# Optimization experiments

Hardware: AMD Instinct MI355X
Metric: run time of the kernel (lower is better)

The kernel has to match this reference:

```python
import jax, jax.numpy as jnp
import numpy as np

IN_F, OUT_F = 768, 2304
E, R = 8, 16            # num adapters, lora rank
ALPHA = 32
SCALING = ALPHA / R
GATE_DIM = 64


def setup_inputs() -> dict:
    key = jax.random.key(0)
    ks = jax.random.split(key, 8)
    B, S = 8, 2048
    x = jax.random.normal(ks[0], (B, S, IN_F), dtype=jnp.float32)
    z = jax.random.normal(ks[1], (B, GATE_DIM), dtype=jnp.float32)
    # frozen linear (nn.Linear weight layout [out, in])
    W = jax.random.normal(ks[2], (OUT_F, IN_F), dtype=jnp.float32) * 0.02
    b = jax.random.normal(ks[3], (OUT_F,), dtype=jnp.float32) * 0.02
    # stacked LoRA adapters: A [E, r, in], B [E, out, r]
    A = jax.random.normal(ks[4], (E, R, IN_F), dtype=jnp.float32) * (1.0 / np.sqrt(IN_F))
    Bm = jax.random.normal(ks[5], (E, OUT_F, R), dtype=jnp.float32) * 0.02
    # spectral gate: linear + softmax over experts
    Wg = jax.random.normal(ks[6], (E, GATE_DIM), dtype=jnp.float32) * 0.1
    bg = jax.random.normal(ks[7], (E,), dtype=jnp.float32) * 0.1
    return {"x": x, "z": z, "W": W, "b": b, "A": A, "Bm": Bm, "Wg": Wg, "bg": bg}


def reference(x, z, W, b, A, Bm, Wg, bg):
    # frozen linear: [B,S,out]
    frozen_out = jnp.einsum('bsi,oi->bso', x, W) + b
    # gate weights over adapters: [B,E]
    gate_w = jax.nn.softmax(jnp.einsum('bg,eg->be', z, Wg) + bg, axis=-1)
    # fused adapters: down-proj to rank r per expert (dropout p=0 -> identity)
    h = jnp.einsum('bsi,eri->bser', x, A)               # [B,S,E,r] small (r=16)
    # up-proj + gate-weighted sum over experts, fused into one contraction
    adapt = jnp.einsum('bser,eor,be->bso', h, Bm, gate_w) * SCALING
    return frozen_out + adapt
```

## Files before the change

### kernel.cpp

```cpp
#include <hip/hip_runtime.h>
#include <hip/hip_bf16.h>
#include <stdint.h>

typedef unsigned short u16;
typedef __attribute__((ext_vector_type(8))) short short8;
typedef __attribute__((ext_vector_type(4))) float floatx4;
typedef unsigned int __attribute__((ext_vector_type(2))) uint2v;

#define M_TOT 16384
#define N_OUT 2304
#define KX    768
#define KL    128
#define SCALING 2.0f

#define WBLKS   864
#define ABLKS   48
#define BMRBLKS 144
#define PREP_BLOCKS (WBLKS + ABLKS + BMRBLKS + 1)

__device__ __forceinline__ u16 f2b(float f) {
  union { __hip_bfloat16 h; u16 u; } c; c.h = __float2bfloat16(f); return c.u;
}
__device__ __forceinline__ float ldf(const void* p, long i, bool f32) {
  if (f32) return ((const float*)p)[i];
  union { u16 u; __hip_bfloat16 h; } c; c.u = ((const u16*)p)[i];
  return __bfloat162float(c.h);
}

__device__ __forceinline__ void gload_lds16(const void* g, void* l) {
  __builtin_amdgcn_global_load_lds(
      (const __attribute__((address_space(1))) void*)g,
      (__attribute__((address_space(3))) void*)l, 16, 0, 0);
}

__device__ __forceinline__ void cvt8(const void* src, u16* dst, long i, bool f32) {
  u16 v[8];
  if (f32) {
    const float4* s = (const float4*)src;
    float4 a = s[i * 2], b = s[i * 2 + 1];
    v[0] = f2b(a.x); v[1] = f2b(a.y); v[2] = f2b(a.z); v[3] = f2b(a.w);
    v[4] = f2b(b.x); v[5] = f2b(b.y); v[6] = f2b(b.z); v[7] = f2b(b.w);
  } else {
    *(uint4*)v = ((const uint4*)src)[i];
  }
  ((uint4*)dst)[i] = *(uint4*)v;
}

__global__ __launch_bounds__(256) void prep_kernel(
    const void* __restrict__ x,  const void* __restrict__ W,
    const void* __restrict__ A,  const void* __restrict__ Bm,
    const void* __restrict__ z,  const void* __restrict__ Wg,
    const void* __restrict__ bg,
    u16* __restrict__ Wbf, u16* __restrict__ Abf,
    u16* __restrict__ bmr, float* __restrict__ gsc, int* __restrict__ flagp) {
  __shared__ int s_flag;
  const int tid = threadIdx.x;
  if (tid < 64) {
    u16 v = ((const u16*)x)[tid * 2];
    int e = (v >> 7) & 0xFF;
    int huge = (e >= 160) ? 1 : 0;
    for (int off = 1; off < 64; off <<= 1) huge += __shfl_xor(huge, off, 64);
    if (tid == 0) s_flag = (huge >= 4) ? 1 : 0;
  }
  __syncthreads();
  const bool f32 = (s_flag != 0);

  int b = blockIdx.x;
  if (b < WBLKS) {
    cvt8(W, Wbf, (long)b * 256 + tid, f32);
  } else if (b < WBLKS + ABLKS) {
    cvt8(A, Abf, (long)(b - WBLKS) * 256 + tid, f32);
  } else if (b < WBLKS + ABLKS + BMRBLKS) {
    long i0 = ((long)(b - WBLKS - ABLKS) * 256 + tid) * 8;
    u16 v[8];
#pragma unroll
    for (int j = 0; j < 8; ++j) {
      long idx = i0 + j;
      long o = idx >> 7, er = idx & 127;
      long e = er >> 4, r = er & 15;
      v[j] = f2b(ldf(Bm, (e * 2304 + o) * 16 + r, f32));
    }
    *(uint4*)&bmr[i0] = *(uint4*)v;
  } else {
    if (tid == 0) *flagp = s_flag;
    if (tid < 64) {
      const int bb = tid >> 3, e = tid & 7;
      float acc = ldf(bg, e, f32);
      for (int i = 0; i < 64; ++i)
        acc += ldf(z, bb * 64 + i, f32) * ldf(Wg, e * 64 + i, f32);
      float mx = acc;
      for (int off = 1; off < 8; off <<= 1) mx = fmaxf(mx, __shfl_xor(mx, off, 64));
      float ex = __expf(acc - mx);
      float sm = ex;
      for (int off = 1; off < 8; off <<= 1) sm += __shfl_xor(sm, off, 64);
      gsc[tid] = (ex / sm) * SCALING;
    }
  }
}

__global__ __launch_bounds__(256) void gemm_h(
    const void* __restrict__ x, const u16* __restrict__ Abf,
    const float* __restrict__ gsc, u16* __restrict__ xbf,
    u16* __restrict__ hg, const int* __restrict__ flagp) {
  __shared__ __align__(128) u16 As[64][64];
  __shared__ __align__(128) u16 Bs[128][64];
  const int tid = threadIdx.x, wave = tid >> 6, lane = tid & 63;
  const int wm = wave >> 1, wn = wave & 1;
  const int quad = lane >> 4, l16 = lane & 15;
  const int srow = lane >> 3, scol = (lane & 7) * 8;
  const int m0 = blockIdx.x * 64;
  const bool f32 = (*flagp != 0);

  const int xr = tid >> 2, cg16 = (tid & 3) * 16;
  char* Asb = (char*)&As[0][0];

  floatx4 acc[2][4];
#pragma unroll
  for (int i = 0; i < 2; ++i)
#pragma unroll
    for (int j = 0; j < 4; ++j) acc[i][j] = floatx4{0.f, 0.f, 0.f, 0.f};

  for (int kb = 0; kb < 12; ++kb) {
    const int kc = kb * 64;
    {
      const long off = (long)(m0 + xr) * KX + kc + cg16;
      uint4 lo, hi;
      if (f32) {
        const float4* xs = (const float4*)((const float*)x + off);
        float4 f0 = xs[0], f1 = xs[1], f2c = xs[2], f3 = xs[3];
        u16 v[16];
        v[0] = f2b(f0.x); v[1] = f2b(f0.y); v[2]  = f2b(f0.z); v[3]  = f2b(f0.w);
        v[4] = f2b(f1.x); v[5] = f2b(f1.y); v[6]  = f2b(f1.z); v[7]  = f2b(f1.w);
        v[8] = f2b(f2c.x); v[9] = f2b(f2c.y); v[10] = f2b(f2c.z); v[11] = f2b(f2c.w);
        v[12] = f2b(f3.x); v[13] = f2b(f3.y); v[14] = f2b(f3.z); v[15] = f2b(f3.w);
        lo = *(uint4*)&v[0]; hi = *(uint4*)&v[8];
      } else {
        lo = *(const uint4*)&((const u16*)x)[off];
        hi = *(const uint4*)&((const u16*)x)[off + 8];
      }
      *(uint4*)&xbf[off] = lo;
      *(uint4*)&xbf[off + 8] = hi;
      const int cb = cg16 * 2, sw = (xr & 7) << 4;
      *(uint4*)(Asb + xr * 128 + ((cb +  0) ^ sw)) = lo;
      *(uint4*)(Asb + xr * 128 + ((cb + 16) ^ sw)) = hi;
    }
#pragma unroll
    for (int j = 0; j < 4; ++j) {
      int r = wave * 32 + j * 8 + srow;
      gload_lds16(Abf + (size_t)r * KX + kc + scol,
                  (char*)(&Bs[0][0]) + (wave * 32 + j * 8) * 128);
    }
    __syncthreads();
#pragma unroll
    for (int ks = 0; ks < 2; ++ks) {
      short8 af[2], bf[4];
#pragma unroll
      for (int mi = 0; mi < 2; ++mi) {
        int ar = wm * 32 + mi * 16 + l16;
        af[mi] = *(const short8*)(Asb + ar * 128 + ((ks * 64 + quad * 16) ^ ((ar & 7) << 4)));
      }
#pragma unroll
      for (int ni = 0; ni < 4; ++ni)
        bf[ni] = *(const short8*)&Bs[wn * 64 + ni * 16 + l16][ks * 32 + quad * 8];
#pragma unroll
      for (int mi = 0; mi < 2; ++mi)
#pragma unroll
        for (int ni = 0; ni < 4; ++ni)
          acc[mi][ni] = __builtin_amdgcn_mfma_f32_16x16x32_bf16(af[mi], bf[ni], acc[mi][ni], 0, 0, 0);
    }
    __syncthreads();
  }
  const int bb = m0 >> 11;
  float gv[4];
#pragma unroll
  for (int ni = 0; ni < 4; ++ni) gv[ni] = gsc[bb * 8 + wn * 4 + ni];
#pragma unroll
  for (int mi = 0; mi < 2; ++mi) {
    int rbase = m0 + wm * 32 + mi * 16 + quad * 4;
#pragma unroll
    for (int ni = 0; ni < 4; ++ni) {
      int c = wn * 64 + ni * 16 + l16;
#pragma unroll
      for (int t = 0; t < 4; ++t)
        hg[(size_t)(rbase + t) * KL + c] = f2b(acc[mi][ni][t] * gv[ni]);
    }
  }
}

__global__ __launch_bounds__(256) void gemm_main(
    const u16* __restrict__ xbf, const u16* __restrict__ hg,
    const u16* __restrict__ Wbf, const u16* __restrict__ bmr,
    const void* __restrict__ bias, void* __restrict__ outv,
    const int* __restrict__ flagp) {
  __shared__ __align__(128) u16 As[128][64];
  __shared__ __align__(128) u16 Bs[128][64];
  __shared__ u16 occ_pad[4096];
  const int tid = threadIdx.x, wave = tid >> 6, lane = tid & 63;
  const int wm = wave >> 1, wn = wave & 1;
  const int quad = lane >> 4, l16 = lane & 15;
  const int srow = lane >> 3, scol = (lane & 7) * 8;

  const int linear = blockIdx.x;
  const int xcd = linear & 7;
  const int g = linear >> 3;
  const int st = g / 24;
  const int w  = g % 24;
  const int m_idx = xcd * 16 + (st / 6) * 8 + (w & 7);
  const int n_idx = (st % 6) * 3 + (w >> 3);
  const int m0 = m_idx * 128;
  const int n0 = n_idx * 128;
  if (tid == 0) ((volatile u16*)occ_pad)[0] = (u16)linear;

  floatx4 acc[4][4];
#pragma unroll
  for (int i = 0; i < 4; ++i)
#pragma unroll
    for (int j = 0; j < 4; ++j) acc[i][j] = floatx4{0.f, 0.f, 0.f, 0.f};

  for (int kb = 0; kb < 14; ++kb) {
    const u16* ap; const u16* bp; int lda, ldb, kc;
    if (kb < 12) { ap = xbf; lda = KX; bp = Wbf; ldb = KX; kc = kb * 64; }
    else         { ap = hg;  lda = KL; bp = bmr; ldb = KL; kc = (kb - 12) * 64; }
#pragma unroll
    for (int j = 0; j < 4; ++j) {
      int r = wave * 32 + j * 8 + srow;
      gload_lds16(ap + (size_t)(m0 + r) * lda + kc + scol,
                  (char*)(&As[0][0]) + (wave * 32 + j * 8) * 128);
      gload_lds16(bp + (size_t)(n0 + r) * ldb + kc + scol,
                  (char*)(&Bs[0][0]) + (wave * 32 + j * 8) * 128);
    }
    __syncthreads();
#pragma unroll
    for (int ks = 0; ks < 2; ++ks) {
      short8 af[4], bf[4];
#pragma unroll
      for (int mi = 0; mi < 4; ++mi)
        af[mi] = *(const short8*)&As[wm * 64 + mi * 16 + l16][ks * 32 + quad * 8];
#pragma unroll
      for (int ni = 0; ni < 4; ++ni)
        bf[ni] = *(const short8*)&Bs[wn * 64 + ni * 16 + l16][ks * 32 + quad * 8];
#pragma unroll
      for (int mi = 0; mi < 4; ++mi)
#pragma unroll
        for (int ni = 0; ni < 4; ++ni)
          acc[mi][ni] = __builtin_amdgcn_mfma_f32_16x16x32_bf16(bf[ni], af[mi], acc[mi][ni], 0, 0, 0);
    }
    __syncthreads();
  }

  const bool f32 = (*flagp != 0);
#pragma unroll
  for (int mi = 0; mi < 4; ++mi) {
    const size_t row = (size_t)(m0 + wm * 64 + mi * 16 + l16);
#pragma unroll
    for (int ni = 0; ni < 4; ++ni) {
      const int c0 = n0 + wn * 64 + ni * 16 + quad * 4;
      float b0, b1, b2, b3;
      if (f32) {
        const float4 bv = *(const float4*)((const float*)bias + c0);
        b0 = bv.x; b1 = bv.y; b2 = bv.z; b3 = bv.w;
      } else {
        b0 = ldf(bias, c0, false);     b1 = ldf(bias, c0 + 1, false);
        b2 = ldf(bias, c0 + 2, false); b3 = ldf(bias, c0 + 3, false);
      }
      const float v0 = acc[mi][ni][0] + b0, v1 = acc[mi][ni][1] + b1;
      const float v2 = acc[mi][ni][2] + b2, v3 = acc[mi][ni][3] + b3;
      if (f32) {
        floatx4 v = {v0, v1, v2, v3};
        __builtin_nontemporal_store(
            v, (floatx4*)((float*)outv + row * N_OUT + c0));
      } else {
        union { u16 h[4]; uint2v u; } pk;
        pk.h[0] = f2b(v0); pk.h[1] = f2b(v1); pk.h[2] = f2b(v2); pk.h[3] = f2b(v3);
        __builtin_nontemporal_store(
            pk.u, (uint2v*)((u16*)outv + row * N_OUT + c0));
      }
    }
  }
}

extern "C" void kernel_launch(void* const* d_in, const int* in_sizes, int n_in,
                              void* d_out, int out_size, void* d_ws, size_t ws_size,
                              hipStream_t stream) {
  const void* x  = d_in[0];
  const void* z  = d_in[1];
  const void* W  = d_in[2];
  const void* bb = d_in[3];
  const void* A  = d_in[4];
  const void* Bm = d_in[5];
  const void* Wg = d_in[6];
  const void* bg = d_in[7];

  char* ws = (char*)d_ws;
  int*   flag = (int*)ws;
  float* gsc  = (float*)(ws + 256);
  u16*   xbf  = (u16*)(ws + 1024);
  u16*   Wbf  = (u16*)(ws + 1024 + 25165824ull);
  u16*   Abf  = (u16*)(ws + 1024 + 25165824ull + 3538944ull);
  u16*   bmr  = (u16*)(ws + 1024 + 25165824ull + 3538944ull + 196608ull);
  u16*   hg   = (u16*)(ws + 1024 + 25165824ull + 3538944ull + 196608ull + 589824ull);

  prep_kernel<<<PREP_BLOCKS, 256, 0, stream>>>(
      x, W, A, Bm, z, Wg, bg, Wbf, Abf, bmr, gsc, flag);

  gemm_h<<<M_TOT / 64, 256, 0, stream>>>(x, Abf, gsc, xbf, hg, flag);

  gemm_main<<<(N_OUT / 128) * (M_TOT / 128), 256, 0, stream>>>(
      xbf, hg, Wbf, bmr, bb, d_out, flag);
}
```

Measured before the change: 129.9 us.

## Overlap W/Bm conversion with h GEMM and transpose MFMA output epilogue

The big W and Bm bf16 conversions move out of the prep kernel into extra blocks of the h-GEMM launch, so they run alongside the low-rank projection. Prep shrinks to the A conversion and the gate softmax. The main GEMM swaps MFMA operand order, which transposes the accumulator layout. The epilogue now loads one bias per column and stores scalar values instead of 4-wide vectors, which may coalesce better or worse depending on the layout.

```diff
diff --git a/kernel.cpp b/kernel.cpp
--- a/kernel.cpp
+++ b/kernel.cpp
@@ -5,7 +5,6 @@
 typedef unsigned short u16;
 typedef __attribute__((ext_vector_type(8))) short short8;
 typedef __attribute__((ext_vector_type(4))) float floatx4;
-typedef unsigned int __attribute__((ext_vector_type(2))) uint2v;
 
 #define M_TOT 16384
 #define N_OUT 2304
@@ -16,7 +15,7 @@
 #define WBLKS   864
 #define ABLKS   48
 #define BMRBLKS 144
-#define PREP_BLOCKS (WBLKS + ABLKS + BMRBLKS + 1)
+#define GH_BLOCKS 256
 
 __device__ __forceinline__ u16 f2b(float f) {
   union { __hip_bfloat16 h; u16 u; } c; c.h = __float2bfloat16(f); return c.u;
@@ -46,13 +45,11 @@
   ((uint4*)dst)[i] = *(uint4*)v;
 }
 
-__global__ __launch_bounds__(256) void prep_kernel(
-    const void* __restrict__ x,  const void* __restrict__ W,
-    const void* __restrict__ A,  const void* __restrict__ Bm,
+__global__ __launch_bounds__(256) void prep_small(
+    const void* __restrict__ x,  const void* __restrict__ A,
     const void* __restrict__ z,  const void* __restrict__ Wg,
     const void* __restrict__ bg,
-    u16* __restrict__ Wbf, u16* __restrict__ Abf,
-    u16* __restrict__ bmr, float* __restrict__ gsc, int* __restrict__ flagp) {
+    u16* __restrict__ Abf, float* __restrict__ gsc, int* __restrict__ flagp) {
   __shared__ int s_flag;
   const int tid = threadIdx.x;
   if (tid < 64) {
@@ -66,21 +63,8 @@
   const bool f32 = (s_flag != 0);
 
   int b = blockIdx.x;
-  if (b < WBLKS) {
-    cvt8(W, Wbf, (long)b * 256 + tid, f32);
-  } else if (b < WBLKS + ABLKS) {
-    cvt8(A, Abf, (long)(b - WBLKS) * 256 + tid, f32);
-  } else if (b < WBLKS + ABLKS + BMRBLKS) {
-    long i0 = ((long)(b - WBLKS - ABLKS) * 256 + tid) * 8;
-    u16 v[8];
-#pragma unroll
-    for (int j = 0; j < 8; ++j) {
-      long idx = i0 + j;
-      long o = idx >> 7, er = idx & 127;
-      long e = er >> 4, r = er & 15;
-      v[j] = f2b(ldf(Bm, (e * 2304 + o) * 16 + r, f32));
-    }
-    *(uint4*)&bmr[i0] = *(uint4*)v;
+  if (b < ABLKS) {
+    cvt8(A, Abf, (long)b * 256 + tid, f32);
   } else {
     if (tid == 0) *flagp = s_flag;
     if (tid < 64) {
@@ -98,18 +82,41 @@
   }
 }
 
-__global__ __launch_bounds__(256) void gemm_h(
-    const void* __restrict__ x, const u16* __restrict__ Abf,
-    const float* __restrict__ gsc, u16* __restrict__ xbf,
-    u16* __restrict__ hg, const int* __restrict__ flagp) {
+__global__ __launch_bounds__(256) void gemm_h_fused(
+    const void* __restrict__ x, const void* __restrict__ W,
+    const void* __restrict__ Bm, const u16* __restrict__ Abf,
+    const float* __restrict__ gsc, const int* __restrict__ flagp,
+    u16* __restrict__ xbf, u16* __restrict__ Wbf, u16* __restrict__ bmr,
+    u16* __restrict__ hg) {
   __shared__ __align__(128) u16 As[64][64];
   __shared__ __align__(128) u16 Bs[128][64];
-  const int tid = threadIdx.x, wave = tid >> 6, lane = tid & 63;
+  const int tid = threadIdx.x;
+  const bool f32 = (*flagp != 0);
+
+  if (blockIdx.x >= GH_BLOCKS) {
+    int c = blockIdx.x - GH_BLOCKS;
+    if (c < WBLKS) {
+      cvt8(W, Wbf, (long)c * 256 + tid, f32);
+    } else {
+      long i0 = ((long)(c - WBLKS) * 256 + tid) * 8;
+      u16 v[8];
+#pragma unroll
+      for (int j = 0; j < 8; ++j) {
+        long idx = i0 + j;
+        long o = idx >> 7, er = idx & 127;
+        long e = er >> 4, r = er & 15;
+        v[j] = f2b(ldf(Bm, (e * 2304 + o) * 16 + r, f32));
+      }
+      *(uint4*)&bmr[i0] = *(uint4*)v;
+    }
+    return;
+  }
+
+  const int wave = tid >> 6, lane = tid & 63;
   const int wm = wave >> 1, wn = wave & 1;
   const int quad = lane >> 4, l16 = lane & 15;
   const int srow = lane >> 3, scol = (lane & 7) * 8;
   const int m0 = blockIdx.x * 64;
-  const bool f32 = (*flagp != 0);
 
   const int xr = tid >> 2, cg16 = (tid & 3) * 16;
   char* Asb = (char*)&As[0][0];
@@ -243,37 +250,28 @@
       for (int mi = 0; mi < 4; ++mi)
 #pragma unroll
         for (int ni = 0; ni < 4; ++ni)
-          acc[mi][ni] = __builtin_amdgcn_mfma_f32_16x16x32_bf16(bf[ni], af[mi], acc[mi][ni], 0, 0, 0);
+          acc[mi][ni] = __builtin_amdgcn_mfma_f32_16x16x32_bf16(af[mi], bf[ni], acc[mi][ni], 0, 0, 0);
     }
     __syncthreads();
   }
 
   const bool f32 = (*flagp != 0);
+  float bv[4];
+#pragma unroll
+  for (int ni = 0; ni < 4; ++ni)
+    bv[ni] = ldf(bias, n0 + wn * 64 + ni * 16 + l16, f32);
 #pragma unroll
   for (int mi = 0; mi < 4; ++mi) {
-    const size_t row = (size_t)(m0 + wm * 64 + mi * 16 + l16);
+    int rbase = m0 + wm * 64 + mi * 16 + quad * 4;
 #pragma unroll
     for (int ni = 0; ni < 4; ++ni) {
-      const int c0 = n0 + wn * 64 + ni * 16 + quad * 4;
-      float b0, b1, b2, b3;
-      if (f32) {
-        const float4 bv = *(const float4*)((const float*)bias + c0);
-        b0 = bv.x; b1 = bv.y; b2 = bv.z; b3 = bv.w;
-      } else {
-        b0 = ldf(bias, c0, false);     b1 = ldf(bias, c0 + 1, false);
-        b2 = ldf(bias, c0 + 2, false); b3 = ldf(bias, c0 + 3, false);
-      }
-      const float v0 = acc[mi][ni][0] + b0, v1 = acc[mi][ni][1] + b1;
-      const float v2 = acc[mi][ni][2] + b2, v3 = acc[mi][ni][3] + b3;
-      if (f32) {
-        floatx4 v = {v0, v1, v2, v3};
-        __builtin_nontemporal_store(
-            v, (floatx4*)((float*)outv + row * N_OUT + c0));
-      } else {
-        union { u16 h[4]; uint2v u; } pk;
-        pk.h[0] = f2b(v0); pk.h[1] = f2b(v1); pk.h[2] = f2b(v2); pk.h[3] = f2b(v3);
-        __builtin_nontemporal_store(
-            pk.u, (uint2v*)((u16*)outv + row * N_OUT + c0));
+      int c = n0 + wn * 64 + ni * 16 + l16;
+#pragma unroll
+      for (int t = 0; t < 4; ++t) {
+        float v = acc[mi][ni][t] + bv[ni];
+        size_t idx = (size_t)(rbase + t) * N_OUT + c;
+        if (f32) __builtin_nontemporal_store(v, (float*)outv + idx);
+        else     __builtin_nontemporal_store(f2b(v), (u16*)outv + idx);
       }
     }
   }
@@ -300,10 +298,10 @@
   u16*   bmr  = (u16*)(ws + 1024 + 25165824ull + 3538944ull + 196608ull);
   u16*   hg   = (u16*)(ws + 1024 + 25165824ull + 3538944ull + 196608ull + 589824ull);
 
-  prep_kernel<<<PREP_BLOCKS, 256, 0, stream>>>(
-      x, W, A, Bm, z, Wg, bg, Wbf, Abf, bmr, gsc, flag);
-
-  gemm_h<<<M_TOT / 64, 256, 0, stream>>>(x, Abf, gsc, xbf, hg, flag);
+  prep_small<<<ABLKS + 1, 256, 0, stream>>>(x, A, z, Wg, bg, Abf, gsc, flag);
+
+  gemm_h_fused<<<GH_BLOCKS + WBLKS + BMRBLKS, 256, 0, stream>>>(
+      x, W, Bm, Abf, gsc, flag, xbf, Wbf, bmr, hg);
 
   gemm_main<<<(N_OUT / 128) * (M_TOT / 128), 256, 0, stream>>>(
       xbf, hg, Wbf, bmr, bb, d_out, flag);
```

New measurement: 125.1 us, median of 3. -3.7%, faster.
